# Kernel tuning notes

Measured on AMD Instinct MI355X. Metric: run time of the kernel, lower is better.

The kernel has to match this reference:

```python
import jax, jax.numpy as jnp
import numpy as np

B = 65536
NUM_INPUTS = 128
H0, H1 = 512, 512
K = 200
MIN_W = 0.001
MIN_H = 0.001
MIN_D = 0.001
EDGE_CONST = float(np.log(np.exp(1.0 - 0.001) - 1.0))  # in-place edge derivative value
LN_EPS = 1e-5


def setup_inputs() -> dict:
    key = jax.random.key(0)
    ks = jax.random.split(key, 10)
    f32 = jnp.float32
    inputs = jax.random.normal(ks[0], (B, NUM_INPUTS), dtype=f32)
    W1 = jax.random.normal(ks[1], (H0, NUM_INPUTS), dtype=f32) / np.sqrt(NUM_INPUTS)
    b1 = jnp.zeros((H0,), f32)
    g1 = jnp.ones((H0,), f32)
    be1 = jnp.zeros((H0,), f32)
    W2 = jax.random.normal(ks[2], (H1, H0), dtype=f32) / np.sqrt(H0)
    b2 = jnp.zeros((H1,), f32)
    g2 = jnp.ones((H1,), f32)
    be2 = jnp.zeros((H1,), f32)
    WV = jax.random.normal(ks[3], (3 * K - 1, H1), dtype=f32) / np.sqrt(H1)
    bV = jnp.zeros((3 * K - 1,), f32)
    Wa = jax.random.normal(ks[4], (1, H1), dtype=f32) / np.sqrt(H1)
    ba = jnp.zeros((1,), f32)
    Wb = jax.random.normal(ks[5], (1, H1), dtype=f32) / np.sqrt(H1)
    bb = jnp.zeros((1,), f32)
    return {"inputs": inputs, "W1": W1, "b1": b1, "g1": g1, "be1": be1,
            "W2": W2, "b2": b2, "g2": g2, "be2": be2,
            "WV": WV, "bV": bV, "Wa": Wa, "ba": ba, "Wb": Wb, "bb": bb}


def _layernorm(x, g, b):
    m = jnp.mean(x, axis=-1, keepdims=True)
    v = jnp.mean(jnp.square(x - m), axis=-1, keepdims=True)
    return (x - m) * jax.lax.rsqrt(v + LN_EPS) * g + b


def _spline_forward(inputs, W1, b1, g1, be1, W2, b2, g2, be2, WV, bV, Wa, ba, Wb, bb):
    x = jax.nn.relu(_layernorm(inputs @ W1.T + b1, g1, be1))
    x = jax.nn.relu(_layernorm(x @ W2.T + b2, g2, be2))
    sp = x @ WV.T + bV                      # [B, 3K-1]
    scale_a = jnp.exp(x @ Wa.T + ba)        # [B, 1]
    scale_b = x @ Wb.T + bb                 # [B, 1]

    Wp = jax.nn.softmax(sp[:, :K], axis=1)
    Hp = jax.nn.softmax(sp[:, K:2 * K], axis=1)
    Dp = sp[:, 2 * K:]                      # [B, K-1]
    Wp = MIN_W + (1.0 - MIN_W * K) * Wp
    Hp = MIN_H + (1.0 - MIN_H * K) * Hp
    Dp = MIN_D + jax.nn.softplus(Dp)
    bsz = inputs.shape[0]
    edge = jnp.full((bsz, 1), EDGE_CONST, dtype=inputs.dtype)
    D = jnp.concatenate([edge, Dp, edge], axis=-1)          # [B, K+1]

    zero = jnp.zeros((bsz, 1), dtype=inputs.dtype)
    cw = jnp.concatenate([zero, jnp.cumsum(Wp, axis=-1)], axis=-1)
    cw = cw.at[:, -1].set(1.0)                              # [B, K+1]
    widths = cw[:, 1:] - cw[:, :-1]                         # [B, K]
    ch = jnp.concatenate([zero, jnp.cumsum(Hp, axis=-1)], axis=-1)
    ch = scale_a * ch + scale_b                             # [B, K+1]
    heights = ch[:, 1:] - ch[:, :-1]                        # [B, K]

    tau = ((jnp.arange(K, dtype=inputs.dtype) + 0.5) / K)   # [K]
    tau = jnp.broadcast_to(tau, (bsz, K))

    # sum(tau >= bins) - 1 == searchsorted(bins, tau, side='right') - 1
    bin_idx = jax.vmap(lambda b, t: jnp.searchsorted(b, t, side='right'))(cw, tau) - 1

    ta = lambda a: jnp.take_along_axis(a, bin_idx, axis=-1)
    in_cw = ta(cw)
    in_w = ta(widths)
    in_ch = ta(ch)
    in_h = ta(heights)
    in_delta = ta(heights / widths)
    d0 = ta(D)
    d1 = ta(D[:, 1:])

    theta = (tau - in_cw) / in_w
    t1mt = theta * (1.0 - theta)
    numer = in_h * (in_delta * jnp.square(theta) + d0 * t1mt)
    denom = in_delta + (d0 + d1 - 2.0 * in_delta) * t1mt
    return in_ch + numer / denom            # [B, K]


def reference(inputs, W1, b1, g1, be1, W2, b2, g2, be2, WV, bV, Wa, ba, Wb, bb):
    return _spline_forward(inputs, W1, b1, g1, be1, W2, b2, g2, be2, WV, bV, Wa, ba, Wb, bb)
```

## Files before the change

### kernel.cpp

```cpp
#include <hip/hip_runtime.h>
#include <stdint.h>

typedef __bf16 bf16;
typedef __bf16 bf16x8 __attribute__((ext_vector_type(8)));
typedef __bf16 bf16x4 __attribute__((ext_vector_type(4)));
typedef float  f32x4  __attribute__((ext_vector_type(4)));
typedef uint32_t u32;

#define BATCH    65536
#define NCAT     640
#define SPSTRIDE 604

#define MFMA __builtin_amdgcn_mfma_f32_16x16x32_bf16

__device__ __forceinline__ void async16(const void* g, void* l) {
    __builtin_amdgcn_global_load_lds(
        (const u32 __attribute__((address_space(1)))*)g,
        (u32 __attribute__((address_space(3)))*)l,
        16, 0, 0);
}

__global__ __launch_bounds__(256) void prep_kernel(
    const float* W1, const float* W2, const float* WV,
    const float* bV, const float* Wa, const float* ba,
    const float* Wb, const float* bb, const float* inputs,
    bf16* w1b, bf16* w2b, bf16* wcat, float* bcat, bf16* xin)
{
    int idx = blockIdx.x * 256 + threadIdx.x;
    const int n1 = 512 * 128, n2 = 512 * 512, n3 = NCAT * 512;
    const int n5 = BATCH * 128 / 8;
    if (idx < n5) {
        const float4* src = (const float4*)(inputs + idx * 8);
        float4 v0 = src[0], v1 = src[1];
        bf16x8 h;
        h[0]=(bf16)v0.x; h[1]=(bf16)v0.y; h[2]=(bf16)v0.z; h[3]=(bf16)v0.w;
        h[4]=(bf16)v1.x; h[5]=(bf16)v1.y; h[6]=(bf16)v1.z; h[7]=(bf16)v1.w;
        *(bf16x8*)&xin[idx * 8] = h;
        return;
    }
    idx -= n5;
    if (idx < n1) { w1b[idx] = (bf16)W1[idx]; return; }
    idx -= n1;
    if (idx < n2) { w2b[idx] = (bf16)W2[idx]; return; }
    idx -= n2;
    if (idx < n3) {
        int n = idx >> 9, k = idx & 511;
        float v = 0.f;
        if (n < 599)       v = WV[n * 512 + k];
        else if (n == 599) v = Wa[k];
        else if (n == 600) v = Wb[k];
        wcat[idx] = (bf16)v;
        return;
    }
    idx -= n3;
    if (idx < NCAT) {
        float v = 0.f;
        if (idx < 599)       v = bV[idx];
        else if (idx == 599) v = ba[0];
        else if (idx == 600) v = bb[0];
        bcat[idx] = v;
    }
}

template <int KDIM>
__global__ __launch_bounds__(1024, 4) void gemm_ln(
    const bf16* __restrict__ A, const bf16* __restrict__ W,
    const float* __restrict__ bias, const float* __restrict__ gamma,
    const float* __restrict__ beta, bf16* out)
{
    __shared__ __align__(16) char smem[65536];
    __shared__ float Psum[128][4], Psq[128][4];

    const int t = threadIdx.x;
    const int lane = t & 63, wid = t >> 6;
    const int wm = wid >> 2, wn = wid & 3;
    const int l16 = lane & 15, g16 = lane >> 4;
    const long row0 = (long)blockIdx.x * 128;
    constexpr int NT = KDIM / 32;

    const bf16* arow0 = A + (row0 + wm * 32 + l16) * (long)KDIM + g16 * 8;
    const bf16* arow1 = arow0 + 16 * KDIM;

    f32x4 acc[2][8];
#pragma unroll
    for (int a = 0; a < 2; ++a)
#pragma unroll
        for (int b = 0; b < 8; ++b) acc[a][b] = (f32x4){0.f, 0.f, 0.f, 0.f};

    auto stageB = [&](int kt, int bi) {
#pragma unroll
        for (int c = 0; c < 2; ++c) {
            int call = c * 16 + wid;
            int row = call * 16 + (lane >> 2);
            const bf16* src = W + (long)row * KDIM + kt * 32 + (lane & 3) * 8;
            async16(src, smem + bi * 32768 + call * 1024);
        }
    };

    stageB(0, 0);
    bf16x8 af0 = *(const bf16x8*)(arow0);
    bf16x8 af1 = *(const bf16x8*)(arow1);
    __syncthreads();

    for (int kt = 0; kt < NT; ++kt) {
        const int bi = kt & 1;
        bf16x8 a0 = af0, a1 = af1;
        if (kt + 1 < NT) {
            stageB(kt + 1, bi ^ 1);
            af0 = *(const bf16x8*)(arow0 + (kt + 1) * 32);
            af1 = *(const bf16x8*)(arow1 + (kt + 1) * 32);
        }
        const bf16* Bb = (const bf16*)(smem + bi * 32768);
#pragma unroll
        for (int fn = 0; fn < 8; ++fn) {
            bf16x8 bv = *(const bf16x8*)(Bb + (wn * 128 + fn * 16 + l16) * 32 + g16 * 8);
            acc[0][fn] = MFMA(a0, bv, acc[0][fn], 0, 0, 0);
            acc[1][fn] = MFMA(a1, bv, acc[1][fn], 0, 0, 0);
        }
        __syncthreads();
    }

    float gv[8], bev[8];
#pragma unroll
    for (int fn = 0; fn < 8; ++fn) {
        int col = wn * 128 + fn * 16 + l16;
        float bv = bias[col];
        gv[fn] = gamma[col]; bev[fn] = beta[col];
#pragma unroll
        for (int fm = 0; fm < 2; ++fm)
#pragma unroll
            for (int i = 0; i < 4; ++i) acc[fm][fn][i] += bv;
    }
#pragma unroll
    for (int fm = 0; fm < 2; ++fm)
#pragma unroll
        for (int i = 0; i < 4; ++i) {
            float s = 0.f, q = 0.f;
#pragma unroll
            for (int fn = 0; fn < 8; ++fn) { float v = acc[fm][fn][i]; s += v; q += v * v; }
#pragma unroll
            for (int m = 1; m < 16; m <<= 1) { s += __shfl_xor(s, m); q += __shfl_xor(q, m); }
            if (l16 == 0) {
                int lr = wm * 32 + fm * 16 + g16 * 4 + i;
                Psum[lr][wn] = s; Psq[lr][wn] = q;
            }
        }
    __syncthreads();
    float mmean[2][4], mrstd[2][4];
#pragma unroll
    for (int fm = 0; fm < 2; ++fm)
#pragma unroll
        for (int i = 0; i < 4; ++i) {
            int lr = wm * 32 + fm * 16 + g16 * 4 + i;
            float s = Psum[lr][0] + Psum[lr][1] + Psum[lr][2] + Psum[lr][3];
            float q = Psq[lr][0] + Psq[lr][1] + Psq[lr][2] + Psq[lr][3];
            float mean = s * (1.f / 512.f);
            float var  = q * (1.f / 512.f) - mean * mean;
            mmean[fm][i] = mean;
            mrstd[fm][i] = rsqrtf(var + 1e-5f);
        }
    bf16* stg = (bf16*)smem;
#pragma unroll
    for (int h = 0; h < 2; ++h) {
        __syncthreads();
#pragma unroll
        for (int fm = 0; fm < 2; ++fm)
#pragma unroll
            for (int i = 0; i < 4; ++i) {
                int lr = wm * 32 + fm * 16 + g16 * 4 + i;
                if ((lr >> 6) != h) continue;
#pragma unroll
                for (int fn = 0; fn < 8; ++fn) {
                    int col = wn * 128 + fn * 16 + l16;
                    float o = (acc[fm][fn][i] - mmean[fm][i]) * mrstd[fm][i] * gv[fn] + bev[fn];
                    stg[(lr & 63) * 512 + col] = (bf16)fmaxf(o, 0.f);
                }
            }
        __syncthreads();
#pragma unroll
        for (int it = 0; it < 4; ++it) {
            int idx = it * 1024 + t;
            *(bf16x8*)&out[(row0 + h * 64 + (idx >> 6)) * 512 + (idx & 63) * 8] =
                *(const bf16x8*)&stg[idx * 8];
        }
    }
}

__global__ __launch_bounds__(1024, 4) void gemm_cat(
    const bf16* __restrict__ A, const bf16* __restrict__ W,
    const float* __restrict__ bcat, bf16* __restrict__ sp, float* __restrict__ ab)
{
    __shared__ __align__(16) char smem[81920];

    const int t = threadIdx.x;
    const int lane = t & 63, wid = t >> 6;
    const int wm = wid >> 2, wn = wid & 3;
    const int l16 = lane & 15, g16 = lane >> 4;
    const long row0 = (long)blockIdx.x * 128;

    const bf16* arow0 = A + (row0 + wm * 32 + l16) * 512 + g16 * 8;
    const bf16* arow1 = arow0 + 16 * 512;

    f32x4 acc[2][10];
#pragma unroll
    for (int a = 0; a < 2; ++a)
#pragma unroll
        for (int b = 0; b < 10; ++b) acc[a][b] = (f32x4){0.f, 0.f, 0.f, 0.f};

    auto stageB = [&](int kt, int bi) {
#pragma unroll
        for (int c = 0; c < 3; ++c) {
            int call = c * 16 + wid;
            if (call < 40) {
                int row = call * 16 + (lane >> 2);
                const bf16* src = W + (long)row * 512 + kt * 32 + (lane & 3) * 8;
                async16(src, smem + bi * 40960 + call * 1024);
            }
        }
    };

    stageB(0, 0);
    bf16x8 af0 = *(const bf16x8*)(arow0);
    bf16x8 af1 = *(const bf16x8*)(arow1);
    __syncthreads();

    for (int kt = 0; kt < 16; ++kt) {
        const int bi = kt & 1;
        bf16x8 a0 = af0, a1 = af1;
        if (kt < 15) {
            stageB(kt + 1, bi ^ 1);
            af0 = *(const bf16x8*)(arow0 + (kt + 1) * 32);
            af1 = *(const bf16x8*)(arow1 + (kt + 1) * 32);
        }
        const bf16* Bb = (const bf16*)(smem + bi * 40960);
#pragma unroll
        for (int fn = 0; fn < 10; ++fn) {
            bf16x8 bv = *(const bf16x8*)(Bb + (wn * 160 + fn * 16 + l16) * 32 + g16 * 8);
            acc[0][fn] = MFMA(a0, bv, acc[0][fn], 0, 0, 0);
            acc[1][fn] = MFMA(a1, bv, acc[1][fn], 0, 0, 0);
        }
        __syncthreads();
    }

    float bv[10];
#pragma unroll
    for (int fn = 0; fn < 10; ++fn) bv[fn] = bcat[wn * 160 + fn * 16 + l16];

#pragma unroll
    for (int fn = 0; fn < 10; ++fn) {
        int col = wn * 160 + fn * 16 + l16;
        if (col == 599 || col == 600) {
#pragma unroll
            for (int fm = 0; fm < 2; ++fm)
#pragma unroll
                for (int i = 0; i < 4; ++i) {
                    int lr = wm * 32 + fm * 16 + g16 * 4 + i;
                    ab[(row0 + lr) * 2 + (col - 599)] = acc[fm][fn][i] + bv[fn];
                }
        }
    }

    bf16* stg = (bf16*)smem;
#pragma unroll
    for (int h = 0; h < 2; ++h) {
        __syncthreads();
#pragma unroll
        for (int fn = 0; fn < 10; ++fn) {
            int col = wn * 160 + fn * 16 + l16;
            if (col >= SPSTRIDE) continue;
#pragma unroll
            for (int fm = 0; fm < 2; ++fm)
#pragma unroll
                for (int i = 0; i < 4; ++i) {
                    int lr = wm * 32 + fm * 16 + g16 * 4 + i;
                    if ((lr >> 6) != h) continue;
                    stg[(lr & 63) * SPSTRIDE + col] = (bf16)(acc[fm][fn][i] + bv[fn]);
                }
        }
        __syncthreads();
#pragma unroll
        for (int it = 0; it < 10; ++it) {
            int c = it * 1024 + t;
            if (c < 64 * 151) {
                int r = c / 151, k = c - r * 151;
                *(uint64_t*)&sp[(row0 + h * 64 + r) * SPSTRIDE + k * 4] =
                    *(const uint64_t*)&stg[r * SPSTRIDE + k * 4];
            }
        }
    }
}

__global__ __launch_bounds__(256) void spline_kernel(
    const bf16* __restrict__ sp, const float* __restrict__ ab, float* __restrict__ out)
{
    __shared__ float S[4][816];
    const int t = threadIdx.x;
    const int lane = t & 63, wid = t >> 6;
    const long row = (long)blockIdx.x * 4 + wid;
    const bf16* spr = sp + row * SPSTRIDE;
    const bool act = lane < 50;
    const float EC = 0.53974247f;
    float* cw = &S[wid][0];
    float* ch = &S[wid][204];
    float* dd = &S[wid][408];
    int*   bx = (int*)&S[wid][612];

    const float sa = __expf(ab[row * 2 + 0]);
    const float sb = ab[row * 2 + 1];

    auto rng = [](float x) -> int {
        int v = (int)ceilf(fmaf(200.f, x, -0.5f));
        return v < 0 ? 0 : (v > 200 ? 200 : v);
    };

    float p0, p1, p2, p3;
    {
        float x0, x1, x2v, x3;
        if (act) {
            bf16x4 v = *(const bf16x4*)&spr[4 * lane];
            x0 = (float)v[0]; x1 = (float)v[1]; x2v = (float)v[2]; x3 = (float)v[3];
        } else { x0 = x1 = x2v = x3 = -1e30f; }
        float m = fmaxf(fmaxf(x0, x1), fmaxf(x2v, x3));
#pragma unroll
        for (int d = 1; d < 64; d <<= 1) m = fmaxf(m, __shfl_xor(m, d));
        float e0 = act ? __expf(x0 - m) : 0.f;
        float e1 = act ? __expf(x1 - m) : 0.f;
        float e2 = act ? __expf(x2v - m) : 0.f;
        float e3 = act ? __expf(x3 - m) : 0.f;
        float s = e0 + e1 + e2 + e3;
#pragma unroll
        for (int d = 1; d < 64; d <<= 1) s += __shfl_xor(s, d);
        float inv = 0.8f / s;
        p0 = act ? fmaf(e0, inv, 0.001f) : 0.f;
        p1 = act ? fmaf(e1, inv, 0.001f) : 0.f;
        p2 = act ? fmaf(e2, inv, 0.001f) : 0.f;
        p3 = act ? fmaf(e3, inv, 0.001f) : 0.f;
    }
    float c0 = p0, c1 = c0 + p1, c2 = c1 + p2, c3 = c2 + p3;
    float run = c3, ts = run;
#pragma unroll
    for (int d = 1; d < 64; d <<= 1) { float u = __shfl_up(ts, d); if (lane >= d) ts += u; }
    float excl  = ts - run;
    float nexcl = __shfl_down(excl, 1);
    float cwl0 = excl, cwl1 = excl + c0, cwl2 = excl + c1, cwl3 = excl + c2;

    float hp0, hp1, hp2, hp3;
    {
        float x0, x1, x2v, x3;
        if (act) {
            bf16x4 v = *(const bf16x4*)&spr[200 + 4 * lane];
            x0 = (float)v[0]; x1 = (float)v[1]; x2v = (float)v[2]; x3 = (float)v[3];
        } else { x0 = x1 = x2v = x3 = -1e30f; }
        float m = fmaxf(fmaxf(x0, x1), fmaxf(x2v, x3));
#pragma unroll
        for (int d = 1; d < 64; d <<= 1) m = fmaxf(m, __shfl_xor(m, d));
        float e0 = act ? __expf(x0 - m) : 0.f;
        float e1 = act ? __expf(x1 - m) : 0.f;
        float e2 = act ? __expf(x2v - m) : 0.f;
        float e3 = act ? __expf(x3 - m) : 0.f;
        float s = e0 + e1 + e2 + e3;
#pragma unroll
        for (int d = 1; d < 64; d <<= 1) s += __shfl_xor(s, d);
        float inv = 0.8f / s;
        hp0 = act ? fmaf(e0, inv, 0.001f) : 0.f;
        hp1 = act ? fmaf(e1, inv, 0.001f) : 0.f;
        hp2 = act ? fmaf(e2, inv, 0.001f) : 0.f;
        hp3 = act ? fmaf(e3, inv, 0.001f) : 0.f;
    }
    float hc0 = hp0, hc1 = hc0 + hp1, hc2 = hc1 + hp2, hc3 = hc2 + hp3;
    float hrun = hc3, hts = hrun;
#pragma unroll
    for (int d = 1; d < 64; d <<= 1) { float u = __shfl_up(hts, d); if (lane >= d) hts += u; }
    float hexcl = hts - hrun;
    float ch0 = fmaf(sa, hexcl, sb);
    float ch1 = fmaf(sa, hexcl + hc0, sb);
    float ch2 = fmaf(sa, hexcl + hc1, sb);
    float ch3 = fmaf(sa, hexcl + hc2, sb);

    float dv0, dv1, dv2, dv3;
    {
        float x0 = 0.f, x1 = 0.f, x2v = 0.f, x3 = 0.f;
        if (act) {
            bf16x4 v = *(const bf16x4*)&spr[400 + 4 * lane];
            x0 = (float)v[0]; x1 = (float)v[1]; x2v = (float)v[2]; x3 = (float)v[3];
        }
        auto spls = [](float x) {
            return fmaxf(x, 0.f) + __logf(1.f + __expf(-fabsf(x))) + 0.001f;
        };
        dv0 = spls(x0); dv1 = spls(x1); dv2 = spls(x2v); dv3 = spls(x3);
    }
    if (lane == 49) dv3 = EC;
    float dprev = __shfl_up(dv3, 1);
    if (lane == 0) dprev = EC;

    if (act) {
        *(f32x4*)&cw[4 * lane] = (f32x4){cwl0, cwl1, cwl2, cwl3};
        *(f32x4*)&ch[4 * lane] = (f32x4){ch0, ch1, ch2, ch3};
        *(f32x4*)&dd[4 * lane] = (f32x4){dprev, dv0, dv1, dv2};
    }
    if (lane == 49) {
        cw[200] = 1.0f;
        ch[200] = fmaf(sa, hts, sb);
        dd[200] = EC;
    }

    if (act) {
        int b0 = rng(cwl0), b1 = rng(cwl1), b2 = rng(cwl2), b3 = rng(cwl3);
        int b4 = (lane == 49) ? 200 : rng(nexcl);
        for (int j = b0; j < b1; ++j) bx[j] = 4 * lane;
        for (int j = b1; j < b2; ++j) bx[j] = 4 * lane + 1;
        for (int j = b2; j < b3; ++j) bx[j] = 4 * lane + 2;
        for (int j = b3; j < b4; ++j) bx[j] = 4 * lane + 3;
    }
    asm volatile("s_waitcnt lgkmcnt(0)" ::: "memory");

    if (act) {
        float* orow = out + (size_t)row * 200;
#pragma unroll
        for (int k = 0; k < 4; ++k) {
            int j = lane + 50 * k;
            int b = bx[j];
            float wl = cw[b], wr = cw[b + 1];
            float hl = ch[b], hr = ch[b + 1];
            float d0 = dd[b], d1 = dd[b + 1];
            float tau = ((float)j + 0.5f) * (1.f / 200.f);
            float w = wr - wl, h = hr - hl;
            float invw = 1.f / w;
            float delta = h * invw;
            float th = (tau - wl) * invw;
            float t1 = th * (1.f - th);
            float numer = h * fmaf(delta * th, th, d0 * t1);
            float denom = fmaf(d0 + d1 - 2.f * delta, t1, delta);
            orow[j] = hl + numer / denom;
        }
    }
}

extern "C" void kernel_launch(void* const* d_in, const int* in_sizes, int n_in,
                              void* d_out, int out_size, void* d_ws, size_t ws_size,
                              hipStream_t stream)
{
    const float* inputs = (const float*)d_in[0];
    const float* W1  = (const float*)d_in[1];
    const float* b1  = (const float*)d_in[2];
    const float* g1  = (const float*)d_in[3];
    const float* be1 = (const float*)d_in[4];
    const float* W2  = (const float*)d_in[5];
    const float* b2  = (const float*)d_in[6];
    const float* g2  = (const float*)d_in[7];
    const float* be2 = (const float*)d_in[8];
    const float* WV  = (const float*)d_in[9];
    const float* bV  = (const float*)d_in[10];
    const float* Wa  = (const float*)d_in[11];
    const float* ba  = (const float*)d_in[12];
    const float* Wb  = (const float*)d_in[13];
    const float* bb  = (const float*)d_in[14];
    float* out = (float*)d_out;

    char* ws = (char*)d_ws;
    bf16*  w1b  = (bf16*) (ws + 0);
    bf16*  w2b  = (bf16*) (ws + 131072);
    bf16*  wcat = (bf16*) (ws + 655360);
    float* bcat = (float*)(ws + 1310720);
    float* ab   = (float*)(ws + 1313280);
    bf16*  x    = (bf16*) (ws + 2097152);
    bf16*  spb  = (bf16*) (ws + 69206016);
    bf16*  xin  = (bf16*) (ws + 69206016);

    const int preptot = BATCH * 128 / 8 + 512 * 128 + 512 * 512 + NCAT * 512 + NCAT;
    prep_kernel<<<(preptot + 255) / 256, 256, 0, stream>>>(
        W1, W2, WV, bV, Wa, ba, Wb, bb, inputs, w1b, w2b, wcat, bcat, xin);

    gemm_ln<128><<<BATCH / 128, 1024, 0, stream>>>(xin, w1b, b1, g1, be1, x);
    gemm_ln<512><<<BATCH / 128, 1024, 0, stream>>>(x,   w2b, b2, g2, be2, x);
    gemm_cat<<<BATCH / 128, 1024, 0, stream>>>(x, wcat, bcat, spb, ab);
    spline_kernel<<<BATCH / 4, 256, 0, stream>>>(spb, ab, out);
}
```

Baseline: 266.2 us.

## Fuse spline evaluation into the head GEMM and relax per-iteration barriers

Merges the concatenated-head GEMM and the spline kernel into one kernel. Each 64-row block keeps its spline parameters in LDS and evaluates the spline directly, so the bf16 sp intermediate and the scale vector no longer make a round trip through global memory. The GEMM main loops also replace __syncthreads with an explicit vmcnt wait plus s_barrier so the next A-fragment prefetch can stay in flight. The costs are smaller blocks (512 threads, 64 rows) with spline work done serially per wave, and a reliance on hand-counted outstanding loads that could break ordering if the compiler emits loads differently.

```diff
diff --git a/kernel.cpp b/kernel.cpp
--- a/kernel.cpp
+++ b/kernel.cpp
@@ -7,11 +7,11 @@
 typedef float  f32x4  __attribute__((ext_vector_type(4)));
 typedef uint32_t u32;
 
-#define BATCH    65536
-#define NCAT     640
-#define SPSTRIDE 604
+#define BATCH 65536
+#define NCAT  640
 
 #define MFMA __builtin_amdgcn_mfma_f32_16x16x32_bf16
+#define FENCE() asm volatile("" ::: "memory")
 
 __device__ __forceinline__ void async16(const void* g, void* l) {
     __builtin_amdgcn_global_load_lds(
@@ -98,15 +98,17 @@
     };
 
     stageB(0, 0);
+    FENCE();
     bf16x8 af0 = *(const bf16x8*)(arow0);
     bf16x8 af1 = *(const bf16x8*)(arow1);
-    __syncthreads();
+    asm volatile("s_waitcnt vmcnt(2)\n\ts_barrier" ::: "memory");
 
     for (int kt = 0; kt < NT; ++kt) {
         const int bi = kt & 1;
         bf16x8 a0 = af0, a1 = af1;
         if (kt + 1 < NT) {
             stageB(kt + 1, bi ^ 1);
+            FENCE();
             af0 = *(const bf16x8*)(arow0 + (kt + 1) * 32);
             af1 = *(const bf16x8*)(arow1 + (kt + 1) * 32);
         }
@@ -117,7 +119,8 @@
             acc[0][fn] = MFMA(a0, bv, acc[0][fn], 0, 0, 0);
             acc[1][fn] = MFMA(a1, bv, acc[1][fn], 0, 0, 0);
         }
-        __syncthreads();
+        if (kt + 1 < NT)
+            asm volatile("s_waitcnt vmcnt(2)\n\ts_barrier" ::: "memory");
     }
 
     float gv[8], bev[8];
@@ -186,127 +189,16 @@
     }
 }
 
-__global__ __launch_bounds__(1024, 4) void gemm_cat(
-    const bf16* __restrict__ A, const bf16* __restrict__ W,
-    const float* __restrict__ bcat, bf16* __restrict__ sp, float* __restrict__ ab)
+__device__ __forceinline__ void spline_row(
+    const bf16* spr, float* tab, float a_in, float sb, float* orow, int lane)
 {
-    __shared__ __align__(16) char smem[81920];
-
-    const int t = threadIdx.x;
-    const int lane = t & 63, wid = t >> 6;
-    const int wm = wid >> 2, wn = wid & 3;
-    const int l16 = lane & 15, g16 = lane >> 4;
-    const long row0 = (long)blockIdx.x * 128;
-
-    const bf16* arow0 = A + (row0 + wm * 32 + l16) * 512 + g16 * 8;
-    const bf16* arow1 = arow0 + 16 * 512;
-
-    f32x4 acc[2][10];
-#pragma unroll
-    for (int a = 0; a < 2; ++a)
-#pragma unroll
-        for (int b = 0; b < 10; ++b) acc[a][b] = (f32x4){0.f, 0.f, 0.f, 0.f};
-
-    auto stageB = [&](int kt, int bi) {
-#pragma unroll
-        for (int c = 0; c < 3; ++c) {
-            int call = c * 16 + wid;
-            if (call < 40) {
-                int row = call * 16 + (lane >> 2);
-                const bf16* src = W + (long)row * 512 + kt * 32 + (lane & 3) * 8;
-                async16(src, smem + bi * 40960 + call * 1024);
-            }
-        }
-    };
-
-    stageB(0, 0);
-    bf16x8 af0 = *(const bf16x8*)(arow0);
-    bf16x8 af1 = *(const bf16x8*)(arow1);
-    __syncthreads();
-
-    for (int kt = 0; kt < 16; ++kt) {
-        const int bi = kt & 1;
-        bf16x8 a0 = af0, a1 = af1;
-        if (kt < 15) {
-            stageB(kt + 1, bi ^ 1);
-            af0 = *(const bf16x8*)(arow0 + (kt + 1) * 32);
-            af1 = *(const bf16x8*)(arow1 + (kt + 1) * 32);
-        }
-        const bf16* Bb = (const bf16*)(smem + bi * 40960);
-#pragma unroll
-        for (int fn = 0; fn < 10; ++fn) {
-            bf16x8 bv = *(const bf16x8*)(Bb + (wn * 160 + fn * 16 + l16) * 32 + g16 * 8);
-            acc[0][fn] = MFMA(a0, bv, acc[0][fn], 0, 0, 0);
-            acc[1][fn] = MFMA(a1, bv, acc[1][fn], 0, 0, 0);
-        }
-        __syncthreads();
-    }
-
-    float bv[10];
-#pragma unroll
-    for (int fn = 0; fn < 10; ++fn) bv[fn] = bcat[wn * 160 + fn * 16 + l16];
-
-#pragma unroll
-    for (int fn = 0; fn < 10; ++fn) {
-        int col = wn * 160 + fn * 16 + l16;
-        if (col == 599 || col == 600) {
-#pragma unroll
-            for (int fm = 0; fm < 2; ++fm)
-#pragma unroll
-                for (int i = 0; i < 4; ++i) {
-                    int lr = wm * 32 + fm * 16 + g16 * 4 + i;
-                    ab[(row0 + lr) * 2 + (col - 599)] = acc[fm][fn][i] + bv[fn];
-                }
-        }
-    }
-
-    bf16* stg = (bf16*)smem;
-#pragma unroll
-    for (int h = 0; h < 2; ++h) {
-        __syncthreads();
-#pragma unroll
-        for (int fn = 0; fn < 10; ++fn) {
-            int col = wn * 160 + fn * 16 + l16;
-            if (col >= SPSTRIDE) continue;
-#pragma unroll
-            for (int fm = 0; fm < 2; ++fm)
-#pragma unroll
-                for (int i = 0; i < 4; ++i) {
-                    int lr = wm * 32 + fm * 16 + g16 * 4 + i;
-                    if ((lr >> 6) != h) continue;
-                    stg[(lr & 63) * SPSTRIDE + col] = (bf16)(acc[fm][fn][i] + bv[fn]);
-                }
-        }
-        __syncthreads();
-#pragma unroll
-        for (int it = 0; it < 10; ++it) {
-            int c = it * 1024 + t;
-            if (c < 64 * 151) {
-                int r = c / 151, k = c - r * 151;
-                *(uint64_t*)&sp[(row0 + h * 64 + r) * SPSTRIDE + k * 4] =
-                    *(const uint64_t*)&stg[r * SPSTRIDE + k * 4];
-            }
-        }
-    }
-}
-
-__global__ __launch_bounds__(256) void spline_kernel(
-    const bf16* __restrict__ sp, const float* __restrict__ ab, float* __restrict__ out)
-{
-    __shared__ float S[4][816];
-    const int t = threadIdx.x;
-    const int lane = t & 63, wid = t >> 6;
-    const long row = (long)blockIdx.x * 4 + wid;
-    const bf16* spr = sp + row * SPSTRIDE;
     const bool act = lane < 50;
     const float EC = 0.53974247f;
-    float* cw = &S[wid][0];
-    float* ch = &S[wid][204];
-    float* dd = &S[wid][408];
-    int*   bx = (int*)&S[wid][612];
-
-    const float sa = __expf(ab[row * 2 + 0]);
-    const float sb = ab[row * 2 + 1];
+    float* cw = tab;
+    float* ch = tab + 204;
+    float* dd = tab + 408;
+    int*   bx = (int*)(tab + 612);
+    const float sa = __expf(a_in);
 
     auto rng = [](float x) -> int {
         int v = (int)ceilf(fmaf(200.f, x, -0.5f));
@@ -415,7 +307,6 @@
     asm volatile("s_waitcnt lgkmcnt(0)" ::: "memory");
 
     if (act) {
-        float* orow = out + (size_t)row * 200;
 #pragma unroll
         for (int k = 0; k < 4; ++k) {
             int j = lane + 50 * k;
@@ -432,6 +323,117 @@
             float numer = h * fmaf(delta * th, th, d0 * t1);
             float denom = fmaf(d0 + d1 - 2.f * delta, t1, delta);
             orow[j] = hl + numer / denom;
+        }
+    }
+}
+
+__global__ __launch_bounds__(512, 4) void gemm_cat_spline(
+    const bf16* __restrict__ A, const bf16* __restrict__ W,
+    const float* __restrict__ bcat, float* __restrict__ out)
+{
+    __shared__ __align__(16) char smem[81920];
+
+    const int t = threadIdx.x;
+    const int lane = t & 63, wid = t >> 6;
+    const int l16 = lane & 15, g16 = lane >> 4;
+    const long row0 = (long)blockIdx.x * 64;
+
+    f32x4 acc[4][5];
+#pragma unroll
+    for (int a = 0; a < 4; ++a)
+#pragma unroll
+        for (int b = 0; b < 5; ++b) acc[a][b] = (f32x4){0.f, 0.f, 0.f, 0.f};
+
+    auto stageB = [&](int kt, int bi) {
+#pragma unroll
+        for (int c = 0; c < 5; ++c) {
+            int call = c * 8 + wid;
+            int row = call * 16 + (lane >> 2);
+            const bf16* src = W + (long)row * 512 + kt * 32 + (lane & 3) * 8;
+            async16(src, smem + bi * 40960 + call * 1024);
+        }
+    };
+
+    const bf16* a0p = A + (row0 + l16) * 512 + g16 * 8;
+
+    stageB(0, 0);
+    FENCE();
+    bf16x8 af0 = *(const bf16x8*)(a0p);
+    bf16x8 af1 = *(const bf16x8*)(a0p + 16 * 512);
+    bf16x8 af2 = *(const bf16x8*)(a0p + 32 * 512);
+    bf16x8 af3 = *(const bf16x8*)(a0p + 48 * 512);
+    asm volatile("s_waitcnt vmcnt(4)\n\ts_barrier" ::: "memory");
+
+    for (int kt = 0; kt < 16; ++kt) {
+        const int bi = kt & 1;
+        bf16x8 a0 = af0, a1 = af1, a2 = af2, a3 = af3;
+        if (kt + 1 < 16) {
+            stageB(kt + 1, bi ^ 1);
+            FENCE();
+            const bf16* ap = a0p + (kt + 1) * 32;
+            af0 = *(const bf16x8*)(ap);
+            af1 = *(const bf16x8*)(ap + 16 * 512);
+            af2 = *(const bf16x8*)(ap + 32 * 512);
+            af3 = *(const bf16x8*)(ap + 48 * 512);
+        }
+        const bf16* Bb = (const bf16*)(smem + bi * 40960);
+#pragma unroll
+        for (int fn = 0; fn < 5; ++fn) {
+            bf16x8 bv = *(const bf16x8*)(Bb + (wid * 80 + fn * 16 + l16) * 32 + g16 * 8);
+            acc[0][fn] = MFMA(a0, bv, acc[0][fn], 0, 0, 0);
+            acc[1][fn] = MFMA(a1, bv, acc[1][fn], 0, 0, 0);
+            acc[2][fn] = MFMA(a2, bv, acc[2][fn], 0, 0, 0);
+            acc[3][fn] = MFMA(a3, bv, acc[3][fn], 0, 0, 0);
+        }
+        if (kt + 1 < 16)
+            asm volatile("s_waitcnt vmcnt(4)\n\ts_barrier" ::: "memory");
+    }
+    __syncthreads();
+
+    bf16*  spL = (bf16*)smem;
+    float* tab = (float*)(smem + 38912) + wid * 816;
+    float* abf = (float*)(smem + 65024);
+
+    float bv[5];
+#pragma unroll
+    for (int fn = 0; fn < 5; ++fn) bv[fn] = bcat[wid * 80 + fn * 16 + l16];
+
+#pragma unroll
+    for (int fn = 0; fn < 5; ++fn) {
+        int col = wid * 80 + fn * 16 + l16;
+        if (col == 599 || col == 600) {
+#pragma unroll
+            for (int fm = 0; fm < 4; ++fm)
+#pragma unroll
+                for (int i = 0; i < 4; ++i)
+                    abf[(fm * 16 + g16 * 4 + i) * 2 + (col - 599)] = acc[fm][fn][i] + bv[fn];
+        }
+    }
+
+#pragma unroll
+    for (int h = 0; h < 2; ++h) {
+        if (h) __syncthreads();
+#pragma unroll
+        for (int fm2 = 0; fm2 < 2; ++fm2) {
+#pragma unroll
+            for (int fn = 0; fn < 5; ++fn) {
+                int col = wid * 80 + fn * 16 + l16;
+                if (col < 601) {
+#pragma unroll
+                    for (int i = 0; i < 4; ++i)
+                        spL[(fm2 * 16 + g16 * 4 + i) * 604 + col] =
+                            (bf16)(acc[2 * h + fm2][fn][i] + bv[fn]);
+                }
+            }
+        }
+        __syncthreads();
+#pragma unroll 1
+        for (int rr = 0; rr < 4; ++rr) {
+            int ridx = wid * 4 + rr;
+            int grow = h * 32 + ridx;
+            spline_row(spL + ridx * 604, tab,
+                       abf[grow * 2 + 0], abf[grow * 2 + 1],
+                       out + (size_t)(row0 + grow) * 200, lane);
         }
     }
 }
@@ -462,9 +464,7 @@
     bf16*  w2b  = (bf16*) (ws + 131072);
     bf16*  wcat = (bf16*) (ws + 655360);
     float* bcat = (float*)(ws + 1310720);
-    float* ab   = (float*)(ws + 1313280);
     bf16*  x    = (bf16*) (ws + 2097152);
-    bf16*  spb  = (bf16*) (ws + 69206016);
     bf16*  xin  = (bf16*) (ws + 69206016);
 
     const int preptot = BATCH * 128 / 8 + 512 * 128 + 512 * 512 + NCAT * 512 + NCAT;
@@ -473,6 +473,5 @@
 
     gemm_ln<128><<<BATCH / 128, 1024, 0, stream>>>(xin, w1b, b1, g1, be1, x);
     gemm_ln<512><<<BATCH / 128, 1024, 0, stream>>>(x,   w2b, b2, g2, be2, x);
-    gemm_cat<<<BATCH / 128, 1024, 0, stream>>>(x, wcat, bcat, spb, ab);
-    spline_kernel<<<BATCH / 4, 256, 0, stream>>>(spb, ab, out);
-}
+    gemm_cat_spline<<<BATCH / 64, 512, 0, stream>>>(x, wcat, bcat, out);
+}
```

Measured after the change: 263.9 us. About the same (-0.9%).
